# Kernel optimization log

Measured on AMD Instinct MI355X. Metric: run time of the kernel, lower is better.

## Reference

```python
import jax, jax.numpy as jnp
import numpy as np

N_NODES = 50000
N_EDGES = 640000
D = 128
N_GRAPHS = 64
N_CLASSES = 32
N_LAYERS = 4


def setup_inputs() -> dict:
    key = jax.random.key(0)
    ks = jax.random.split(key, 8)
    x = jax.random.normal(ks[0], (N_NODES, D), dtype=jnp.float32)
    edge_index = jax.random.randint(ks[1], (2, N_EDGES), 0, N_NODES, dtype=jnp.int64)
    batch = jnp.sort(jax.random.randint(ks[2], (N_NODES,), 0, N_GRAPHS, dtype=jnp.int64))
    s = 0.05  # small init scale (stand-in for init_weights)
    w1 = jax.random.normal(ks[3], (N_LAYERS, D, D), dtype=jnp.float32) * s
    b1 = jnp.zeros((N_LAYERS, D), dtype=jnp.float32)
    w2 = jax.random.normal(ks[4], (N_LAYERS, D, D), dtype=jnp.float32) * s
    b2 = jnp.zeros((N_LAYERS, D), dtype=jnp.float32)
    w_lin = jax.random.normal(ks[5], (D, N_CLASSES), dtype=jnp.float32) * s
    b_lin = jnp.zeros((N_CLASSES,), dtype=jnp.float32)
    return {"x": x, "edge_index": edge_index, "batch": batch,
            "w1": w1, "b1": b1, "w2": w2, "b2": b2,
            "w_lin": w_lin, "b_lin": b_lin}


def reference(x, edge_index, batch, w1, b1, w2, b2, w_lin, b_lin):
    # GIN stack: num_layers GINConv layers (eps=0, sum aggregation,
    # MLP = Linear -> ReLU -> Linear), ReLU between layers (not after last).
    src, dst = edge_index[0], edge_index[1]
    n = x.shape[0]
    h = x
    for i in range(N_LAYERS):
        # neighbor sum aggregation: scatter-add messages h[src] into dst
        agg = jax.ops.segment_sum(h[src], dst, num_segments=n)
        z = h + agg  # (1 + eps) * x_i + sum_j x_j, eps = 0
        z = jnp.maximum(z @ w1[i] + b1[i], 0.0)
        h = z @ w2[i] + b2[i]
        if i < N_LAYERS - 1:
            h = jax.nn.relu(h)
    # global_mean_pool over graph ids
    sums = jax.ops.segment_sum(h, batch, num_segments=N_GRAPHS)
    counts = jax.ops.segment_sum(jnp.ones((n,), dtype=h.dtype), batch, num_segments=N_GRAPHS)
    pooled = sums / jnp.maximum(counts, 1.0)[:, None]
    logits = pooled @ w_lin + b_lin
    return (pooled, logits)
```

## Files before the change

### kernel.cpp

```cpp
#include <hip/hip_runtime.h>
#include <hip/hip_fp16.h>


typedef short short8 __attribute__((ext_vector_type(8)));
typedef float floatx4 __attribute__((ext_vector_type(4)));

#define TM 32
#define ZSTRIDE 136

__device__ __forceinline__ unsigned short f2bf(float x) {
    unsigned int u = __float_as_uint(x);
    u += 0x7fffu + ((u >> 16) & 1u);
    return (unsigned short)(u >> 16);
}
__device__ __forceinline__ float bf2f(unsigned short h) {
    return __uint_as_float(((unsigned int)h) << 16);
}

__device__ __forceinline__ float2 ldrowh(const char* __restrict__ base,
                                         int id, unsigned laneoff) {
    __half2 h = *(const __half2*)(base + ((unsigned)id << 8) + laneoff);
    return __half22float2(h);
}


__global__ __launch_bounds__(256) void gin_build1(
    const int* __restrict__ dst, int nEdges, int* __restrict__ counts,
    const float* __restrict__ w1, const float* __restrict__ w2,
    unsigned short* __restrict__ whf, unsigned short* __restrict__ wlf, int wTotal,
    const float* __restrict__ x, __half* __restrict__ xh, int nNodes) {
    const int gsize = gridDim.x * 256;
    const int gtid = blockIdx.x * 256 + threadIdx.x;
    for (int idx = gtid; idx < wTotal; idx += gsize) {
        int mat  = idx >> 14;
        int rem  = idx & 16383;
        int kc   = rem >> 12;
        int ct   = (rem >> 9) & 7;
        int lane = (rem >> 3) & 63;
        int j    = rem & 7;
        int row = kc * 32 + (lane >> 4) * 8 + j;
        int col = ct * 16 + (lane & 15);
        int L = mat >> 1;
        const float* W = (mat & 1) ? (w2 + (size_t)L * 16384) : (w1 + (size_t)L * 16384);
        float v = W[row * 128 + col];
        unsigned short h = f2bf(v);
        unsigned short l = f2bf(v - bf2f(h));
        whf[idx] = h;
        wlf[idx] = l;
    }
    const int total4 = nNodes * 32;
    for (int i = gtid; i < total4; i += gsize) {
        float4 v = ((const float4*)x)[i];
        union { __half2 h[2]; float2 f; } u;
        u.h[0] = __halves2half2(__float2half_rn(v.x), __float2half_rn(v.y));
        u.h[1] = __halves2half2(__float2half_rn(v.z), __float2half_rn(v.w));
        ((float2*)xh)[i] = u.f;
    }
    for (int i = gtid; i < nEdges; i += gsize) atomicAdd(&counts[dst[i]], 1);
}


__global__ __launch_bounds__(256) void gin_scanA(const int* __restrict__ counts,
                                                 int* __restrict__ offsets,
                                                 int* __restrict__ partials, int n) {
    __shared__ int s[256];
    int t = threadIdx.x;
    int i = blockIdx.x * 256 + t;
    int v = (i < n) ? counts[i] : 0;
    s[t] = v;
    __syncthreads();
    for (int off = 1; off < 256; off <<= 1) {
        int u = (t >= off) ? s[t - off] : 0;
        __syncthreads();
        s[t] += u;
        __syncthreads();
    }
    if (i < n) offsets[i] = s[t] - v;
    if (t == 255) partials[blockIdx.x] = s[255];
}


__global__ __launch_bounds__(256) void gin_scanB(int* __restrict__ offsets,
                                                 const int* __restrict__ partials,
                                                 int* __restrict__ cursor,
                                                 int nb, int n, int nEdges) {
    __shared__ int s[256];
    int t = threadIdx.x;
    s[t] = (t < nb) ? partials[t] : 0;
    __syncthreads();
    for (int off = 1; off < 256; off <<= 1) {
        int u = (t >= off) ? s[t - off] : 0;
        __syncthreads();
        s[t] += u;
        __syncthreads();
    }
    int base = (blockIdx.x > 0) ? s[blockIdx.x - 1] : 0;
    int i = blockIdx.x * 256 + t;
    if (i < n) {
        int o = offsets[i] + base;
        offsets[i] = o;
        cursor[i]  = o;
    }
    if (i == 0) offsets[n] = nEdges;
}


__global__ __launch_bounds__(256) void gin_scatter(const int* __restrict__ src,
                                                   const int* __restrict__ dst,
                                                   int nEdges,
                                                   int* __restrict__ cursor,
                                                   int* __restrict__ ssrc) {
    int i = blockIdx.x * 256 + threadIdx.x;
    if (i < nEdges) {
        int p = atomicAdd(&cursor[dst[i]], 1);
        ssrc[p] = src[i];
    }
}


__global__ __launch_bounds__(256) void gin_layer(const __half* __restrict__ hin,
                                                 const int* __restrict__ offs,
                                                 const int* __restrict__ ssrc,
                                                 const unsigned short* __restrict__ whf,
                                                 const unsigned short* __restrict__ wlf,
                                                 int matBase,
                                                 const float* __restrict__ b1p,
                                                 const float* __restrict__ b2p,
                                                 __half* __restrict__ hout,
                                                 const int* __restrict__ batch,
                                                 float* __restrict__ gsums,
                                                 int nNodes, int lastLayer) {
    __shared__ unsigned short smem[2 * TM * ZSTRIDE];
    unsigned short* zh = smem;
    unsigned short* zl = smem + TM * ZSTRIDE;
    const int tid = threadIdx.x;
    const int w = tid >> 6, lane = tid & 63;
    const int lo4 = lane & 15, hi4 = lane >> 4;
    const int rowbase = blockIdx.x * TM;
    const char* hbase = (const char*)hin;
    const unsigned laneoff = (unsigned)lane * 4u;

    const int gbase = rowbase + w * 8;
#pragma unroll
    for (int pp = 0; pp < 4; ++pp) {
        int nA = gbase + 2 * pp, nB = nA + 1;
        bool okA = nA < nNodes, okB = nB < nNodes;
        float2 aA = make_float2(0.f, 0.f), aB = make_float2(0.f, 0.f);
        if (okA) aA = ldrowh(hbase, nA, laneoff);
        if (okB) aB = ldrowh(hbase, nB, laneoff);
        int eA = okA ? offs[nA] : 0, endA = okA ? offs[nA + 1] : 0;
        int eB = okB ? offs[nB] : 0, endB = okB ? offs[nB + 1] : 0;

        while (eA + 4 <= endA && eB + 4 <= endB) {
            int sA0 = ssrc[eA], sA1 = ssrc[eA + 1], sA2 = ssrc[eA + 2], sA3 = ssrc[eA + 3];
            int sB0 = ssrc[eB], sB1 = ssrc[eB + 1], sB2 = ssrc[eB + 2], sB3 = ssrc[eB + 3];
            float2 vA0 = ldrowh(hbase, sA0, laneoff);
            float2 vA1 = ldrowh(hbase, sA1, laneoff);
            float2 vA2 = ldrowh(hbase, sA2, laneoff);
            float2 vA3 = ldrowh(hbase, sA3, laneoff);
            float2 vB0 = ldrowh(hbase, sB0, laneoff);
            float2 vB1 = ldrowh(hbase, sB1, laneoff);
            float2 vB2 = ldrowh(hbase, sB2, laneoff);
            float2 vB3 = ldrowh(hbase, sB3, laneoff);
            aA.x += (vA0.x + vA1.x) + (vA2.x + vA3.x);
            aA.y += (vA0.y + vA1.y) + (vA2.y + vA3.y);
            aB.x += (vB0.x + vB1.x) + (vB2.x + vB3.x);
            aB.y += (vB0.y + vB1.y) + (vB2.y + vB3.y);
            eA += 4; eB += 4;
        }
        for (; eA + 4 <= endA; eA += 4) {
            int s0 = ssrc[eA], s1 = ssrc[eA + 1], s2 = ssrc[eA + 2], s3 = ssrc[eA + 3];
            float2 v0 = ldrowh(hbase, s0, laneoff);
            float2 v1 = ldrowh(hbase, s1, laneoff);
            float2 v2 = ldrowh(hbase, s2, laneoff);
            float2 v3 = ldrowh(hbase, s3, laneoff);
            aA.x += (v0.x + v1.x) + (v2.x + v3.x);
            aA.y += (v0.y + v1.y) + (v2.y + v3.y);
        }
        for (; eA < endA; ++eA) {
            float2 v = ldrowh(hbase, ssrc[eA], laneoff);
            aA.x += v.x; aA.y += v.y;
        }
        for (; eB + 4 <= endB; eB += 4) {
            int s0 = ssrc[eB], s1 = ssrc[eB + 1], s2 = ssrc[eB + 2], s3 = ssrc[eB + 3];
            float2 v0 = ldrowh(hbase, s0, laneoff);
            float2 v1 = ldrowh(hbase, s1, laneoff);
            float2 v2 = ldrowh(hbase, s2, laneoff);
            float2 v3 = ldrowh(hbase, s3, laneoff);
            aB.x += (v0.x + v1.x) + (v2.x + v3.x);
            aB.y += (v0.y + v1.y) + (v2.y + v3.y);
        }
        for (; eB < endB; ++eB) {
            float2 v = ldrowh(hbase, ssrc[eB], laneoff);
            aB.x += v.x; aB.y += v.y;
        }
        int rA = nA - rowbase, rB = rA + 1;
        unsigned short hx = f2bf(aA.x), hy = f2bf(aA.y);
        ((unsigned int*)zh)[rA * (ZSTRIDE / 2) + lane] = (unsigned)hx | ((unsigned)hy << 16);
        ((unsigned int*)zl)[rA * (ZSTRIDE / 2) + lane] =
            (unsigned)f2bf(aA.x - bf2f(hx)) | ((unsigned)f2bf(aA.y - bf2f(hy)) << 16);
        hx = f2bf(aB.x); hy = f2bf(aB.y);
        ((unsigned int*)zh)[rB * (ZSTRIDE / 2) + lane] = (unsigned)hx | ((unsigned)hy << 16);
        ((unsigned int*)zl)[rB * (ZSTRIDE / 2) + lane] =
            (unsigned)f2bf(aB.x - bf2f(hx)) | ((unsigned)f2bf(aB.y - bf2f(hy)) << 16);
    }
    __syncthreads();

    floatx4 acc[2][2];
#pragma unroll
    for (int rg = 0; rg < 2; ++rg)
#pragma unroll
        for (int ct = 0; ct < 2; ++ct) acc[rg][ct] = (floatx4)0.f;

    for (int kc = 0; kc < 4; ++kc) {
        size_t o0 = ((((size_t)matBase * 4 + kc) * 8 + (2 * w)) * 64 + lane) * 8;
        size_t o1 = ((((size_t)matBase * 4 + kc) * 8 + (2 * w + 1)) * 64 + lane) * 8;
        short8 bh0 = *(const short8*)(whf + o0), bl0 = *(const short8*)(wlf + o0);
        short8 bh1 = *(const short8*)(whf + o1), bl1 = *(const short8*)(wlf + o1);
#pragma unroll
        for (int rg = 0; rg < 2; ++rg) {
            const int rbase = (rg * 16 + lo4) * ZSTRIDE + kc * 32 + hi4 * 8;
            short8 ah = *(const short8*)(zh + rbase);
            short8 al = *(const short8*)(zl + rbase);
            acc[rg][0] = __builtin_amdgcn_mfma_f32_16x16x32_bf16(ah, bh0, acc[rg][0], 0, 0, 0);
            acc[rg][0] = __builtin_amdgcn_mfma_f32_16x16x32_bf16(al, bh0, acc[rg][0], 0, 0, 0);
            acc[rg][0] = __builtin_amdgcn_mfma_f32_16x16x32_bf16(ah, bl0, acc[rg][0], 0, 0, 0);
            acc[rg][1] = __builtin_amdgcn_mfma_f32_16x16x32_bf16(ah, bh1, acc[rg][1], 0, 0, 0);
            acc[rg][1] = __builtin_amdgcn_mfma_f32_16x16x32_bf16(al, bh1, acc[rg][1], 0, 0, 0);
            acc[rg][1] = __builtin_amdgcn_mfma_f32_16x16x32_bf16(ah, bl1, acc[rg][1], 0, 0, 0);
        }
    }
    __syncthreads();

    float bb1_0 = b1p[w * 32 + lo4];
    float bb1_1 = b1p[w * 32 + 16 + lo4];
#pragma unroll
    for (int rg = 0; rg < 2; ++rg)
#pragma unroll
        for (int ct = 0; ct < 2; ++ct) {
            float bb = ct ? bb1_1 : bb1_0;
#pragma unroll
            for (int r = 0; r < 4; ++r) {
                float v = fmaxf(acc[rg][ct][r] + bb, 0.f);
                unsigned short h = f2bf(v);
                int idx = (rg * 16 + hi4 * 4 + r) * ZSTRIDE + w * 32 + ct * 16 + lo4;
                zh[idx] = h;
                zl[idx] = f2bf(v - bf2f(h));
            }
        }
    __syncthreads();

#pragma unroll
    for (int rg = 0; rg < 2; ++rg)
#pragma unroll
        for (int ct = 0; ct < 2; ++ct) acc[rg][ct] = (floatx4)0.f;

    for (int kc = 0; kc < 4; ++kc) {
        size_t o0 = ((((size_t)(matBase + 1) * 4 + kc) * 8 + (2 * w)) * 64 + lane) * 8;
        size_t o1 = ((((size_t)(matBase + 1) * 4 + kc) * 8 + (2 * w + 1)) * 64 + lane) * 8;
        short8 bh0 = *(const short8*)(whf + o0), bl0 = *(const short8*)(wlf + o0);
        short8 bh1 = *(const short8*)(whf + o1), bl1 = *(const short8*)(wlf + o1);
#pragma unroll
        for (int rg = 0; rg < 2; ++rg) {
            const int rbase = (rg * 16 + lo4) * ZSTRIDE + kc * 32 + hi4 * 8;
            short8 ah = *(const short8*)(zh + rbase);
            short8 al = *(const short8*)(zl + rbase);
            acc[rg][0] = __builtin_amdgcn_mfma_f32_16x16x32_bf16(ah, bh0, acc[rg][0], 0, 0, 0);
            acc[rg][0] = __builtin_amdgcn_mfma_f32_16x16x32_bf16(al, bh0, acc[rg][0], 0, 0, 0);
            acc[rg][0] = __builtin_amdgcn_mfma_f32_16x16x32_bf16(ah, bl0, acc[rg][0], 0, 0, 0);
            acc[rg][1] = __builtin_amdgcn_mfma_f32_16x16x32_bf16(ah, bh1, acc[rg][1], 0, 0, 0);
            acc[rg][1] = __builtin_amdgcn_mfma_f32_16x16x32_bf16(al, bh1, acc[rg][1], 0, 0, 0);
            acc[rg][1] = __builtin_amdgcn_mfma_f32_16x16x32_bf16(ah, bl1, acc[rg][1], 0, 0, 0);
        }
    }

    float bb2_0 = b2p[w * 32 + lo4];
    float bb2_1 = b2p[w * 32 + 16 + lo4];

    if (!lastLayer) {
#pragma unroll
        for (int rg = 0; rg < 2; ++rg)
#pragma unroll
            for (int ct = 0; ct < 2; ++ct) {
                float bb = ct ? bb2_1 : bb2_0;
#pragma unroll
                for (int r = 0; r < 4; ++r) {
                    int row = rowbase + rg * 16 + hi4 * 4 + r;
                    if (row < nNodes) {
                        float v = fmaxf(acc[rg][ct][r] + bb, 0.f);
                        hout[(size_t)row * 128 + w * 32 + ct * 16 + lo4] = __float2half_rn(v);
                    }
                }
            }
    } else {
        __syncthreads();
        float* zf = (float*)smem;
#pragma unroll
        for (int rg = 0; rg < 2; ++rg)
#pragma unroll
            for (int ct = 0; ct < 2; ++ct) {
                float bb = ct ? bb2_1 : bb2_0;
#pragma unroll
                for (int r = 0; r < 4; ++r)
                    zf[(rg * 16 + hi4 * 4 + r) * 132 + w * 32 + ct * 16 + lo4] =
                        acc[rg][ct][r] + bb;
            }
        __syncthreads();
        int c = tid & 127, half = tid >> 7;
        int rmax = nNodes - rowbase;
        if (rmax > TM) rmax = TM;
        float accp = 0.f;
        int gcur = -1;
        for (int r = half; r < rmax; r += 2) {
            int g = batch[rowbase + r];
            if (g != gcur) {
                if (gcur >= 0) atomicAdd(&gsums[gcur * 128 + c], accp);
                accp = 0.f;
                gcur = g;
            }
            accp += zf[r * 132 + c];
        }
        if (gcur >= 0) atomicAdd(&gsums[gcur * 128 + c], accp);
    }
}


__device__ __forceinline__ int lb_search(const int* __restrict__ a, int n, int key) {
    int lo = 0, hi = n;
    while (lo < hi) {
        int m = (lo + hi) >> 1;
        if (a[m] < key) lo = m + 1; else hi = m;
    }
    return lo;
}

__global__ __launch_bounds__(128) void gin_pool2(const float* __restrict__ gsums,
                                                 const int* __restrict__ batch, int nNodes,
                                                 const float* __restrict__ wlin,
                                                 const float* __restrict__ blin,
                                                 float* __restrict__ out, int nGraphs) {
    __shared__ float sp[128];
    int g = blockIdx.x;
    int t = threadIdx.x;
    int start = lb_search(batch, nNodes, g);
    int end   = lb_search(batch, nNodes, g + 1);
    float cnt = (float)(end - start);
    float p = gsums[(size_t)g * 128 + t] / fmaxf(cnt, 1.0f);
    out[(size_t)g * 128 + t] = p;
    sp[t] = p;
    __syncthreads();
    if (t < 32) {
        float s = blin[t];
        for (int k = 0; k < 128; ++k) s += sp[k] * wlin[k * 32 + t];
        out[(size_t)nGraphs * 128 + g * 32 + t] = s;
    }
}


extern "C" void kernel_launch(void* const* d_in, const int* in_sizes, int n_in,
                              void* d_out, int out_size, void* d_ws, size_t ws_size,
                              hipStream_t stream) {
    const float* x     = (const float*)d_in[0];
    const int*   ei    = (const int*)d_in[1];
    const int*   batch = (const int*)d_in[2];
    const float* w1    = (const float*)d_in[3];
    const float* b1    = (const float*)d_in[4];
    const float* w2    = (const float*)d_in[5];
    const float* b2    = (const float*)d_in[6];
    const float* wlin  = (const float*)d_in[7];
    const float* blin  = (const float*)d_in[8];
    float* out = (float*)d_out;

    const int nNodes  = in_sizes[0] / 128;
    const int nEdges  = in_sizes[1] / 2;
    const int nLayers = in_sizes[3] / (128 * 128);
    const int nGraphs = out_size / 160;

    const int* srcArr = ei;
    const int* dstArr = ei + nEdges;

    char* p = (char*)d_ws;
    int*   counts   = (int*)p;            p += (size_t)nNodes * 4;
    float* gsums    = (float*)p;          p += (size_t)nGraphs * 128 * 4;
    int*   offsets  = (int*)p;            p += (size_t)(nNodes + 1) * 4;
    int*   cursor   = (int*)p;            p += (size_t)nNodes * 4;
    int*   partials = (int*)p;            p += 256 * 4;
    int*   ssrc     = (int*)p;            p += (size_t)nEdges * 4;

    p = (char*)(((uintptr_t)p + 63) & ~(uintptr_t)63);
    const int wTotal = nLayers * 2 * 16384;
    unsigned short* whf = (unsigned short*)p;  p += (size_t)wTotal * 2;
    unsigned short* wlf = (unsigned short*)p;  p += (size_t)wTotal * 2;

    p = (char*)(((uintptr_t)p + 63) & ~(uintptr_t)63);
    __half* xh   = (__half*)p;            p += (size_t)nNodes * 128 * 2;
    __half* bufA = (__half*)p;            p += (size_t)nNodes * 128 * 2;
    __half* bufB = (__half*)p;

    const size_t zeroBytes = ((size_t)nNodes + (size_t)nGraphs * 128) * 4;
    hipMemsetAsync(d_ws, 0, zeroBytes, stream);

    const int eb = (nEdges + 255) / 256;
    const int nb = (nNodes + 255) / 256;

    gin_build1<<<eb, 256, 0, stream>>>(dstArr, nEdges, counts, w1, w2, whf, wlf, wTotal,
                                       x, xh, nNodes);
    gin_scanA<<<nb, 256, 0, stream>>>(counts, offsets, partials, nNodes);
    gin_scanB<<<nb, 256, 0, stream>>>(offsets, partials, cursor, nb, nNodes, nEdges);
    gin_scatter<<<eb, 256, 0, stream>>>(srcArr, dstArr, nEdges, cursor, ssrc);

    const int lb = (nNodes + TM - 1) / TM;
    const __half* hin = xh;
    __half* bufs[2] = {bufA, bufB};
    for (int L = 0; L < nLayers; ++L) {
        int last = (L == nLayers - 1);
        __half* hout = bufs[L & 1];
        gin_layer<<<lb, 256, 0, stream>>>(hin, offsets, ssrc, whf, wlf, 2 * L,
                                          b1 + (size_t)L * 128, b2 + (size_t)L * 128,
                                          hout, batch, gsums, nNodes, last);
        hin = hout;
    }
    gin_pool2<<<nGraphs, 128, 0, stream>>>(gsums, batch, nNodes, wlin, blin, out, nGraphs);
}
```

Before: 323.1 us.

## Use 512-thread blocks in GIN layer with eight waves splitting rows and columns

Doubles the wavefronts per 32-row tile from four to eight. Each wave now gathers neighbour sums for 4 rows instead of 8, and computes a 16-column slice of each MLP matmul instead of 32. The aim is more memory-level parallelism in the latency-bound gather and fewer registers per wave. In exchange, each block loads more weight fragments in total, barriers must sync more waves, and the 512-thread blocks may limit how many blocks fit per CU.

```diff
diff --git a/kernel.cpp b/kernel.cpp
--- a/kernel.cpp
+++ b/kernel.cpp
@@ -118,7 +118,7 @@
 }
 
 
-__global__ __launch_bounds__(256) void gin_layer(const __half* __restrict__ hin,
+__global__ __launch_bounds__(512) void gin_layer(const __half* __restrict__ hin,
                                                  const int* __restrict__ offs,
                                                  const int* __restrict__ ssrc,
                                                  const unsigned short* __restrict__ whf,
@@ -140,9 +140,9 @@
     const char* hbase = (const char*)hin;
     const unsigned laneoff = (unsigned)lane * 4u;
 
-    const int gbase = rowbase + w * 8;
-#pragma unroll
-    for (int pp = 0; pp < 4; ++pp) {
+    const int gbase = rowbase + w * 4;
+#pragma unroll
+    for (int pp = 0; pp < 2; ++pp) {
         int nA = gbase + 2 * pp, nB = nA + 1;
         bool okA = nA < nNodes, okB = nB < nNodes;
         float2 aA = make_float2(0.f, 0.f), aB = make_float2(0.f, 0.f);
@@ -206,90 +206,66 @@
     }
     __syncthreads();
 
-    floatx4 acc[2][2];
-#pragma unroll
-    for (int rg = 0; rg < 2; ++rg)
-#pragma unroll
-        for (int ct = 0; ct < 2; ++ct) acc[rg][ct] = (floatx4)0.f;
+    floatx4 acc[2];
+    acc[0] = (floatx4)0.f;
+    acc[1] = (floatx4)0.f;
 
     for (int kc = 0; kc < 4; ++kc) {
-        size_t o0 = ((((size_t)matBase * 4 + kc) * 8 + (2 * w)) * 64 + lane) * 8;
-        size_t o1 = ((((size_t)matBase * 4 + kc) * 8 + (2 * w + 1)) * 64 + lane) * 8;
-        short8 bh0 = *(const short8*)(whf + o0), bl0 = *(const short8*)(wlf + o0);
-        short8 bh1 = *(const short8*)(whf + o1), bl1 = *(const short8*)(wlf + o1);
+        size_t o = ((((size_t)matBase * 4 + kc) * 8 + w) * 64 + lane) * 8;
+        short8 bh = *(const short8*)(whf + o), bl = *(const short8*)(wlf + o);
 #pragma unroll
         for (int rg = 0; rg < 2; ++rg) {
             const int rbase = (rg * 16 + lo4) * ZSTRIDE + kc * 32 + hi4 * 8;
             short8 ah = *(const short8*)(zh + rbase);
             short8 al = *(const short8*)(zl + rbase);
-            acc[rg][0] = __builtin_amdgcn_mfma_f32_16x16x32_bf16(ah, bh0, acc[rg][0], 0, 0, 0);
-            acc[rg][0] = __builtin_amdgcn_mfma_f32_16x16x32_bf16(al, bh0, acc[rg][0], 0, 0, 0);
-            acc[rg][0] = __builtin_amdgcn_mfma_f32_16x16x32_bf16(ah, bl0, acc[rg][0], 0, 0, 0);
-            acc[rg][1] = __builtin_amdgcn_mfma_f32_16x16x32_bf16(ah, bh1, acc[rg][1], 0, 0, 0);
-            acc[rg][1] = __builtin_amdgcn_mfma_f32_16x16x32_bf16(al, bh1, acc[rg][1], 0, 0, 0);
-            acc[rg][1] = __builtin_amdgcn_mfma_f32_16x16x32_bf16(ah, bl1, acc[rg][1], 0, 0, 0);
-        }
-    }
-    __syncthreads();
-
-    float bb1_0 = b1p[w * 32 + lo4];
-    float bb1_1 = b1p[w * 32 + 16 + lo4];
+            acc[rg] = __builtin_amdgcn_mfma_f32_16x16x32_bf16(ah, bh, acc[rg], 0, 0, 0);
+            acc[rg] = __builtin_amdgcn_mfma_f32_16x16x32_bf16(al, bh, acc[rg], 0, 0, 0);
+            acc[rg] = __builtin_amdgcn_mfma_f32_16x16x32_bf16(ah, bl, acc[rg], 0, 0, 0);
+        }
+    }
+    __syncthreads();
+
+    float bb1 = b1p[w * 16 + lo4];
 #pragma unroll
     for (int rg = 0; rg < 2; ++rg)
 #pragma unroll
-        for (int ct = 0; ct < 2; ++ct) {
-            float bb = ct ? bb1_1 : bb1_0;
-#pragma unroll
-            for (int r = 0; r < 4; ++r) {
-                float v = fmaxf(acc[rg][ct][r] + bb, 0.f);
-                unsigned short h = f2bf(v);
-                int idx = (rg * 16 + hi4 * 4 + r) * ZSTRIDE + w * 32 + ct * 16 + lo4;
-                zh[idx] = h;
-                zl[idx] = f2bf(v - bf2f(h));
-            }
-        }
-    __syncthreads();
-
-#pragma unroll
-    for (int rg = 0; rg < 2; ++rg)
-#pragma unroll
-        for (int ct = 0; ct < 2; ++ct) acc[rg][ct] = (floatx4)0.f;
+        for (int r = 0; r < 4; ++r) {
+            float v = fmaxf(acc[rg][r] + bb1, 0.f);
+            unsigned short h = f2bf(v);
+            int idx = (rg * 16 + hi4 * 4 + r) * ZSTRIDE + w * 16 + lo4;
+            zh[idx] = h;
+            zl[idx] = f2bf(v - bf2f(h));
+        }
+    __syncthreads();
+
+    acc[0] = (floatx4)0.f;
+    acc[1] = (floatx4)0.f;
 
     for (int kc = 0; kc < 4; ++kc) {
-        size_t o0 = ((((size_t)(matBase + 1) * 4 + kc) * 8 + (2 * w)) * 64 + lane) * 8;
-        size_t o1 = ((((size_t)(matBase + 1) * 4 + kc) * 8 + (2 * w + 1)) * 64 + lane) * 8;
-        short8 bh0 = *(const short8*)(whf + o0), bl0 = *(const short8*)(wlf + o0);
-        short8 bh1 = *(const short8*)(whf + o1), bl1 = *(const short8*)(wlf + o1);
+        size_t o = ((((size_t)(matBase + 1) * 4 + kc) * 8 + w) * 64 + lane) * 8;
+        short8 bh = *(const short8*)(whf + o), bl = *(const short8*)(wlf + o);
 #pragma unroll
         for (int rg = 0; rg < 2; ++rg) {
             const int rbase = (rg * 16 + lo4) * ZSTRIDE + kc * 32 + hi4 * 8;
             short8 ah = *(const short8*)(zh + rbase);
             short8 al = *(const short8*)(zl + rbase);
-            acc[rg][0] = __builtin_amdgcn_mfma_f32_16x16x32_bf16(ah, bh0, acc[rg][0], 0, 0, 0);
-            acc[rg][0] = __builtin_amdgcn_mfma_f32_16x16x32_bf16(al, bh0, acc[rg][0], 0, 0, 0);
-            acc[rg][0] = __builtin_amdgcn_mfma_f32_16x16x32_bf16(ah, bl0, acc[rg][0], 0, 0, 0);
-            acc[rg][1] = __builtin_amdgcn_mfma_f32_16x16x32_bf16(ah, bh1, acc[rg][1], 0, 0, 0);
-            acc[rg][1] = __builtin_amdgcn_mfma_f32_16x16x32_bf16(al, bh1, acc[rg][1], 0, 0, 0);
-            acc[rg][1] = __builtin_amdgcn_mfma_f32_16x16x32_bf16(ah, bl1, acc[rg][1], 0, 0, 0);
-        }
-    }
-
-    float bb2_0 = b2p[w * 32 + lo4];
-    float bb2_1 = b2p[w * 32 + 16 + lo4];
+            acc[rg] = __builtin_amdgcn_mfma_f32_16x16x32_bf16(ah, bh, acc[rg], 0, 0, 0);
+            acc[rg] = __builtin_amdgcn_mfma_f32_16x16x32_bf16(al, bh, acc[rg], 0, 0, 0);
+            acc[rg] = __builtin_amdgcn_mfma_f32_16x16x32_bf16(ah, bl, acc[rg], 0, 0, 0);
+        }
+    }
+
+    float bb2 = b2p[w * 16 + lo4];
 
     if (!lastLayer) {
 #pragma unroll
         for (int rg = 0; rg < 2; ++rg)
 #pragma unroll
-            for (int ct = 0; ct < 2; ++ct) {
-                float bb = ct ? bb2_1 : bb2_0;
-#pragma unroll
-                for (int r = 0; r < 4; ++r) {
-                    int row = rowbase + rg * 16 + hi4 * 4 + r;
-                    if (row < nNodes) {
-                        float v = fmaxf(acc[rg][ct][r] + bb, 0.f);
-                        hout[(size_t)row * 128 + w * 32 + ct * 16 + lo4] = __float2half_rn(v);
-                    }
+            for (int r = 0; r < 4; ++r) {
+                int row = rowbase + rg * 16 + hi4 * 4 + r;
+                if (row < nNodes) {
+                    float v = fmaxf(acc[rg][r] + bb2, 0.f);
+                    hout[(size_t)row * 128 + w * 16 + lo4] = __float2half_rn(v);
                 }
             }
     } else {
@@ -298,20 +274,15 @@
 #pragma unroll
         for (int rg = 0; rg < 2; ++rg)
 #pragma unroll
-            for (int ct = 0; ct < 2; ++ct) {
-                float bb = ct ? bb2_1 : bb2_0;
-#pragma unroll
-                for (int r = 0; r < 4; ++r)
-                    zf[(rg * 16 + hi4 * 4 + r) * 132 + w * 32 + ct * 16 + lo4] =
-                        acc[rg][ct][r] + bb;
-            }
-        __syncthreads();
-        int c = tid & 127, half = tid >> 7;
+            for (int r = 0; r < 4; ++r)
+                zf[(rg * 16 + hi4 * 4 + r) * 132 + w * 16 + lo4] = acc[rg][r] + bb2;
+        __syncthreads();
+        int c = tid & 127, q = tid >> 7;
         int rmax = nNodes - rowbase;
         if (rmax > TM) rmax = TM;
         float accp = 0.f;
         int gcur = -1;
-        for (int r = half; r < rmax; r += 2) {
+        for (int r = q; r < rmax; r += 4) {
             int g = batch[rowbase + r];
             if (g != gcur) {
                 if (gcur >= 0) atomicAdd(&gsums[gcur * 128 + c], accp);
@@ -415,7 +386,7 @@
     for (int L = 0; L < nLayers; ++L) {
         int last = (L == nLayers - 1);
         __half* hout = bufs[L & 1];
-        gin_layer<<<lb, 256, 0, stream>>>(hin, offsets, ssrc, whf, wlf, 2 * L,
+        gin_layer<<<lb, 512, 0, stream>>>(hin, offsets, ssrc, whf, wlf, 2 * L,
                                           b1 + (size_t)L * 128, b2 + (size_t)L * 128,
                                           hout, batch, gsums, nNodes, last);
         hin = hout;
```

Result: no change. 327.2 us (+1.3%).

## Fuse CSR build phases into one cooperative kernel with grid syncs

Applied to the files above, without the earlier changes.

Merges the four preprocessing kernels (count/convert, scan A, scan B, scatter) into a single cooperative launch of 1024 blocks that uses grid.sync between phases. The aim is to remove three kernel launch gaps and their drain/refill costs. The non-cooperative path is kept as a fallback if the cooperative launch fails. Grid-wide barriers cost something of their own, and the fixed grid size means each thread handles more elements per loop.

```diff
diff --git a/kernel.cpp b/kernel.cpp
--- a/kernel.cpp
+++ b/kernel.cpp
@@ -1,5 +1,8 @@
 #include <hip/hip_runtime.h>
 #include <hip/hip_fp16.h>
+#include <hip/hip_cooperative_groups.h>
+
+namespace cg = cooperative_groups;
 
 
 typedef short short8 __attribute__((ext_vector_type(8)));
@@ -24,13 +27,12 @@
 }
 
 
-__global__ __launch_bounds__(256) void gin_build1(
-    const int* __restrict__ dst, int nEdges, int* __restrict__ counts,
-    const float* __restrict__ w1, const float* __restrict__ w2,
-    unsigned short* __restrict__ whf, unsigned short* __restrict__ wlf, int wTotal,
+__device__ __forceinline__ void build_phase1(
+    int gtid, int gsize, const int* __restrict__ dst, int nEdges,
+    int* __restrict__ counts, const float* __restrict__ w1,
+    const float* __restrict__ w2, unsigned short* __restrict__ whf,
+    unsigned short* __restrict__ wlf, int wTotal,
     const float* __restrict__ x, __half* __restrict__ xh, int nNodes) {
-    const int gsize = gridDim.x * 256;
-    const int gtid = blockIdx.x * 256 + threadIdx.x;
     for (int idx = gtid; idx < wTotal; idx += gsize) {
         int mat  = idx >> 14;
         int rem  = idx & 16383;
@@ -60,6 +62,79 @@
 }
 
 
+__global__ __launch_bounds__(256) void gin_build(
+    const int* __restrict__ src, const int* __restrict__ dst, int nEdges,
+    int* __restrict__ counts, int* __restrict__ offsets,
+    int* __restrict__ cursor, int* __restrict__ partials,
+    int* __restrict__ ssrc,
+    const float* __restrict__ w1, const float* __restrict__ w2,
+    unsigned short* __restrict__ whf, unsigned short* __restrict__ wlf,
+    int wTotal, const float* __restrict__ x, __half* __restrict__ xh,
+    int nNodes, int nChunks) {
+    cg::grid_group grid = cg::this_grid();
+    const int gsize = gridDim.x * 256;
+    const int gtid = blockIdx.x * 256 + threadIdx.x;
+    const int t = threadIdx.x;
+    __shared__ int s[256];
+
+    build_phase1(gtid, gsize, dst, nEdges, counts, w1, w2, whf, wlf, wTotal,
+                 x, xh, nNodes);
+    grid.sync();
+
+    if (blockIdx.x < (unsigned)nChunks) {
+        int i = blockIdx.x * 256 + t;
+        int v = (i < nNodes) ? counts[i] : 0;
+        s[t] = v;
+        __syncthreads();
+        for (int off = 1; off < 256; off <<= 1) {
+            int u = (t >= off) ? s[t - off] : 0;
+            __syncthreads();
+            s[t] += u;
+            __syncthreads();
+        }
+        if (i < nNodes) offsets[i] = s[t] - v;
+        if (t == 255) partials[blockIdx.x] = s[255];
+    }
+    grid.sync();
+
+    if (blockIdx.x < (unsigned)nChunks) {
+        s[t] = (t < nChunks) ? partials[t] : 0;
+        __syncthreads();
+        for (int off = 1; off < 256; off <<= 1) {
+            int u = (t >= off) ? s[t - off] : 0;
+            __syncthreads();
+            s[t] += u;
+            __syncthreads();
+        }
+        int base = (blockIdx.x > 0) ? s[blockIdx.x - 1] : 0;
+        int i = blockIdx.x * 256 + t;
+        if (i < nNodes) {
+            int o = offsets[i] + base;
+            offsets[i] = o;
+            cursor[i]  = o;
+        }
+        if (i == 0) offsets[nNodes] = nEdges;
+    }
+    grid.sync();
+
+    for (int i = gtid; i < nEdges; i += gsize) {
+        int p = atomicAdd(&cursor[dst[i]], 1);
+        ssrc[p] = src[i];
+    }
+}
+
+
+__global__ __launch_bounds__(256) void gin_build1(
+    const int* __restrict__ dst, int nEdges, int* __restrict__ counts,
+    const float* __restrict__ w1, const float* __restrict__ w2,
+    unsigned short* __restrict__ whf, unsigned short* __restrict__ wlf, int wTotal,
+    const float* __restrict__ x, __half* __restrict__ xh, int nNodes) {
+    const int gsize = gridDim.x * 256;
+    const int gtid = blockIdx.x * 256 + threadIdx.x;
+    build_phase1(gtid, gsize, dst, nEdges, counts, w1, w2, whf, wlf, wTotal,
+                 x, xh, nNodes);
+}
+
 __global__ __launch_bounds__(256) void gin_scanA(const int* __restrict__ counts,
                                                  int* __restrict__ offsets,
                                                  int* __restrict__ partials, int n) {
@@ -79,7 +154,6 @@
     if (t == 255) partials[blockIdx.x] = s[255];
 }
 
-
 __global__ __launch_bounds__(256) void gin_scanB(int* __restrict__ offsets,
                                                  const int* __restrict__ partials,
                                                  int* __restrict__ cursor,
@@ -103,7 +177,6 @@
     }
     if (i == 0) offsets[n] = nEdges;
 }
-
 
 __global__ __launch_bounds__(256) void gin_scatter(const int* __restrict__ src,
                                                    const int* __restrict__ dst,
@@ -403,11 +476,25 @@
     const int eb = (nEdges + 255) / 256;
     const int nb = (nNodes + 255) / 256;
 
-    gin_build1<<<eb, 256, 0, stream>>>(dstArr, nEdges, counts, w1, w2, whf, wlf, wTotal,
-                                       x, xh, nNodes);
-    gin_scanA<<<nb, 256, 0, stream>>>(counts, offsets, partials, nNodes);
-    gin_scanB<<<nb, 256, 0, stream>>>(offsets, partials, cursor, nb, nNodes, nEdges);
-    gin_scatter<<<eb, 256, 0, stream>>>(srcArr, dstArr, nEdges, cursor, ssrc);
+    {
+        int nChunks = nb;
+        void* args[] = {
+            (void*)&srcArr, (void*)&dstArr, (void*)&nEdges,
+            (void*)&counts, (void*)&offsets, (void*)&cursor, (void*)&partials,
+            (void*)&ssrc, (void*)&w1, (void*)&w2, (void*)&whf, (void*)&wlf,
+            (void*)&wTotal, (void*)&x, (void*)&xh, (void*)&nNodes, (void*)&nChunks
+        };
+        hipError_t err = hipLaunchCooperativeKernel(
+            (const void*)gin_build, dim3(1024), dim3(256), args, 0, stream);
+        if (err != hipSuccess) {
+            gin_build1<<<eb, 256, 0, stream>>>(dstArr, nEdges, counts, w1, w2,
+                                               whf, wlf, wTotal, x, xh, nNodes);
+            gin_scanA<<<nb, 256, 0, stream>>>(counts, offsets, partials, nNodes);
+            gin_scanB<<<nb, 256, 0, stream>>>(offsets, partials, cursor, nb,
+                                              nNodes, nEdges);
+            gin_scatter<<<eb, 256, 0, stream>>>(srcArr, dstArr, nEdges, cursor, ssrc);
+        }
+    }
 
     const int lb = (nNodes + TM - 1) / TM;
     const __half* hin = xh;
```

Result: slower. 641.7 us (+98.6%).
